# Kernel tuning notes

Hardware: AMD Instinct MI355X
Metric: run time of the kernel (lower is better)

Reference implementation:

```python
import jax, jax.numpy as jnp
import numpy as np
from jax import lax

# Dims from LSTMTagger class constants
B, S, LP = 1024, 128, 14       # sentences, words/sentence, padded chars/word
K, CE, WE, Lf = 3, 6, 10, 4    # char window, char emb, word emb, cnn filters
H, V, A, T = 6, 50000, 100, 135  # lstm hidden, vocab, alphabet, tagset
D = WE + Lf                     # lstm input dim = 14
LW = LP - K + 1                 # conv windows per word = 12


def setup_inputs() -> dict:
    key = jax.random.key(0)
    ks = jax.random.split(key, 14)
    n = lambda k, shp: jax.random.normal(k, shp, dtype=jnp.float32) * 0.1
    inp = {
        "word_idx": jax.random.randint(ks[0], (B, S), 0, V, dtype=jnp.int32),
        "char_idx": jax.random.randint(ks[1], (B, S, LP), 0, A, dtype=jnp.int32),
        "word_emb": n(ks[2], (V, WE)),
        "char_emb": n(ks[3], (A, CE)),
        "Wc": n(ks[4], (Lf, K * CE)),   # Conv1d(1, l, K*CE) weight, squeezed
        "bc": n(ks[5], (Lf,)),
        "Wih_f": n(ks[6], (4 * H, D)),
        "Whh_f": n(ks[7], (4 * H, H)),
        "b_f": n(ks[8], (4 * H,)),      # b_ih + b_hh fused (equivalent)
        "Wih_b": n(ks[9], (4 * H, D)),
        "Whh_b": n(ks[10], (4 * H, H)),
        "b_b": n(ks[11], (4 * H,)),
        "Wt": n(ks[12], (T, 2 * H)),
        "bt": n(ks[13], (T,)),
    }
    return inp


def _lstm_scan(xs, Wih, Whh, b):
    # xs: [S, B, D] -> hs: [S, B, H]; torch gate order i, f, g, o
    h0 = jnp.zeros((xs.shape[1], H), xs.dtype)

    def step(carry, xt):
        h, c = carry
        g = xt @ Wih.T + h @ Whh.T + b
        i, f, gg, o = jnp.split(g, 4, axis=-1)
        c = jax.nn.sigmoid(f) * c + jax.nn.sigmoid(i) * jnp.tanh(gg)
        h = jax.nn.sigmoid(o) * jnp.tanh(c)
        return (h, c), h

    _, hs = lax.scan(step, (h0, h0), xs)
    return hs


def reference(word_emb, char_emb, Wc, bc, Wih_f, Whh_f, b_f,
              Wih_b, Whh_b, b_b, Wt, bt, word_idx, char_idx):
    # per-word char CNN: sliding K-char windows, flatten, linear, max-pool
    ce = char_emb[char_idx]                              # [B,S,LP,CE]
    windows = jnp.concatenate([ce[:, :, i:i + LW] for i in range(K)], axis=-1)  # [B,S,LW,K*CE]
    phi = jnp.einsum('bswk,lk->bswl', windows, Wc) + bc  # [B,S,LW,Lf]
    char_repr = phi.max(axis=2)                          # [B,S,Lf]

    we = word_emb[word_idx]                              # [B,S,WE]
    x = jnp.concatenate([we, char_repr], axis=-1)        # [B,S,D]

    xs = x.transpose(1, 0, 2)                            # [S,B,D]
    hf = _lstm_scan(xs, Wih_f, Whh_f, b_f)               # forward direction
    hb = _lstm_scan(xs[::-1], Wih_b, Whh_b, b_b)[::-1]   # backward direction
    out = jnp.concatenate([hf, hb], axis=-1).transpose(1, 0, 2)  # [B,S,2H]

    tag_space = out @ Wt.T + bt                          # [B,S,T]
    return jax.nn.log_softmax(tag_space, axis=-1)
```

## Files before the change

kernel.cpp:

```cpp
#include <hip/hip_runtime.h>

#define B_   1024
#define S_   128
#define LP_  14
#define K_   3
#define CE_  6
#define WE_  10
#define LF_  4
#define H_   6
#define D_   14
#define T_   135
#define LW_  12
#define V_   50000
#define A_   100
#define SGST 52

static __device__ __forceinline__ float fsigm(float x) {
    return __frcp_rn(1.0f + __expf(-x));
}
static __device__ __forceinline__ float ftanh(float x) {
    return fmaf(2.0f, __frcp_rn(1.0f + __expf(-2.0f * x)), -1.0f);
}

static __device__ __forceinline__ float wave_sum64(float s) {
    int v = __float_as_int(s);
    float f;
    f = __int_as_float(__builtin_amdgcn_update_dpp(0, v, 0xB1, 0xF, 0xF, true));  s += f; v = __float_as_int(s);
    f = __int_as_float(__builtin_amdgcn_update_dpp(0, v, 0x4E, 0xF, 0xF, true));  s += f; v = __float_as_int(s);
    f = __int_as_float(__builtin_amdgcn_update_dpp(0, v, 0x141, 0xF, 0xF, true)); s += f; v = __float_as_int(s);
    f = __int_as_float(__builtin_amdgcn_update_dpp(0, v, 0x140, 0xF, 0xF, true)); s += f; v = __float_as_int(s);
    f = __int_as_float(__builtin_amdgcn_update_dpp(0, v, 0x142, 0xA, 0xF, true)); s += f; v = __float_as_int(s);
    f = __int_as_float(__builtin_amdgcn_update_dpp(0, v, 0x143, 0xC, 0xF, true)); s += f; v = __float_as_int(s);
    return __int_as_float(__builtin_amdgcn_readlane(v, 63));
}

__global__ __launch_bounds__(128, 2) void k_f(
    const int* __restrict__ word_idx, const int* __restrict__ char_idx,
    const float* __restrict__ word_emb, const float* __restrict__ char_emb,
    const float* __restrict__ Wc, const float* __restrict__ bc,
    const float* __restrict__ Wih_f, const float* __restrict__ Whh_f, const float* __restrict__ b_f,
    const float* __restrict__ Wih_b, const float* __restrict__ Whh_b, const float* __restrict__ b_b,
    float* __restrict__ hbuf)
{
    __shared__ __align__(16) float s_g[S_][SGST];
    __shared__ __align__(16) float s_h[S_][12];
    __shared__ float s_ce[A_ * CE_];
    __shared__ float s_wc[LF_ * K_ * CE_];
    __shared__ float s_bc[LF_];

    int t = threadIdx.x;
    int b = blockIdx.x;

    for (int e = t; e < A_ * CE_; e += 128) s_ce[e] = char_emb[e];
    if (t < LF_ * K_ * CE_) s_wc[t] = Wc[t];
    if (t < LF_) s_bc[t] = bc[t];
    __syncthreads();

    {
        int w = b * S_ + t;
        const int2* ci2 = (const int2*)(char_idx + (size_t)w * LP_);
        int idxs[LP_];
        #pragma unroll
        for (int p = 0; p < 7; ++p) {
            int2 v = ci2[p];
            idxs[2 * p] = v.x; idxs[2 * p + 1] = v.y;
        }
        float ce[LP_][CE_];
        #pragma unroll
        for (int p = 0; p < LP_; ++p) {
            int idx = idxs[p];
            idx = idx < 0 ? 0 : (idx >= A_ ? A_ - 1 : idx);
            #pragma unroll
            for (int c = 0; c < CE_; ++c) ce[p][c] = s_ce[idx * CE_ + c];
        }
        float x[D_];
        #pragma unroll
        for (int l = 0; l < LF_; ++l) {
            float acc[LW_];
            float bl = s_bc[l];
            #pragma unroll
            for (int q = 0; q < LW_; ++q) acc[q] = bl;
            #pragma unroll
            for (int kk = 0; kk < K_; ++kk) {
                #pragma unroll
                for (int c = 0; c < CE_; ++c) {
                    float wv_ = s_wc[l * (K_ * CE_) + kk * CE_ + c];
                    #pragma unroll
                    for (int q = 0; q < LW_; ++q) acc[q] = fmaf(ce[q + kk][c], wv_, acc[q]);
                }
            }
            float m = acc[0];
            #pragma unroll
            for (int q = 1; q < LW_; ++q) m = fmaxf(m, acc[q]);
            x[WE_ + l] = m;
        }
        int wi = word_idx[w];
        wi = wi < 0 ? 0 : (wi >= V_ ? V_ - 1 : wi);
        const float2* wep = (const float2*)(word_emb + (size_t)wi * WE_);
        #pragma unroll
        for (int c = 0; c < WE_ / 2; ++c) {
            float2 v = wep[c];
            x[2 * c] = v.x; x[2 * c + 1] = v.y;
        }

        float4* dstf = (float4*)&s_g[t][0];
        {
            float g[24];
            #pragma unroll
            for (int r = 0; r < 24; ++r) {
                float a = b_f[r];
                #pragma unroll
                for (int k = 0; k < D_; ++k) a = fmaf(Wih_f[r * D_ + k], x[k], a);
                g[r] = a;
            }
            #pragma unroll
            for (int u = 0; u < H_; ++u)
                dstf[u] = make_float4(g[u], g[H_ + u], g[2 * H_ + u], g[3 * H_ + u]);
        }
        float4* dstb = (float4*)&s_g[t][24];
        {
            float g[24];
            #pragma unroll
            for (int r = 0; r < 24; ++r) {
                float a = b_b[r];
                #pragma unroll
                for (int k = 0; k < D_; ++k) a = fmaf(Wih_b[r * D_ + k], x[k], a);
                g[r] = a;
            }
            #pragma unroll
            for (int u = 0; u < H_; ++u)
                dstb[u] = make_float4(g[u], g[H_ + u], g[2 * H_ + u], g[3 * H_ + u]);
        }
    }
    __syncthreads();

    {
        int wv   = t >> 6;
        int lane = t & 63;
        bool act = (lane < H_);
        int u    = act ? lane : (H_ - 1);

        const float* Whh = wv ? Whh_b : Whh_f;
        float w0[H_], w1[H_], w2[H_], w3[H_];
        #pragma unroll
        for (int k = 0; k < H_; ++k) {
            w0[k] = Whh[(0 * H_ + u) * H_ + k];
            w1[k] = Whh[(1 * H_ + u) * H_ + k];
            w2[k] = Whh[(2 * H_ + u) * H_ + k];
            w3[k] = Whh[(3 * H_ + u) * H_ + k];
        }

        const float* gp = &s_g[wv ? (S_ - 1) : 0][wv * 24 + u * 4];
        const int gstep = wv ? -SGST : SGST;

        float h[H_];
        #pragma unroll
        for (int k = 0; k < H_; ++k) h[k] = 0.f;
        float c = 0.f;

        float4 g4 = *(const float4*)gp;

#define LSTEP(G4, J)                                                            \
        {                                                                       \
            float ai = (G4).x, af = (G4).y, ag = (G4).z, ao = (G4).w;           \
            _Pragma("unroll")                                                   \
            for (int k = 0; k < H_; ++k) {                                      \
                ai = fmaf(w0[k], h[k], ai);                                     \
                af = fmaf(w1[k], h[k], af);                                     \
                ag = fmaf(w2[k], h[k], ag);                                     \
                ao = fmaf(w3[k], h[k], ao);                                     \
            }                                                                   \
            float si = fsigm(ai), sf = fsigm(af), so = fsigm(ao), tg = ftanh(ag); \
            c = fmaf(sf, c, si * tg);                                           \
            float hu = so * ftanh(c);                                           \
            int se = wv ? (S_ - 1 - (J)) : (J);                                 \
            if (act) s_h[se][wv * H_ + u] = hu;                                 \
            _Pragma("unroll")                                                   \
            for (int k = 0; k < H_; ++k)                                        \
                h[k] = __int_as_float(__builtin_amdgcn_readlane(__float_as_int(hu), k)); \
        }

        #pragma unroll 4
        for (int j = 0; j < S_ - 1; ++j) {
            gp += gstep;
            float4 nx = *(const float4*)gp;
            LSTEP(g4, j);
            g4 = nx;
        }
        LSTEP(g4, S_ - 1);
#undef LSTEP
    }
    __syncthreads();

    {
        float4* dst = (float4*)(hbuf + (size_t)b * S_ * 12);
        const float4* src = (const float4*)&s_h[0][0];
        #pragma unroll
        for (int i = 0; i < 3; ++i) dst[t + 128 * i] = src[t + 128 * i];
    }
}

__global__ __launch_bounds__(256) void k_p(
    const float* __restrict__ hbuf,
    const float* __restrict__ Wt, const float* __restrict__ bt,
    float* __restrict__ out)
{
    __shared__ float s_hb[64 * 12];
    int t = threadIdx.x;
    int ib = blockIdx.x * 64;
    {
        const float4* src = (const float4*)(hbuf + (size_t)ib * 12);
        float4* dst = (float4*)s_hb;
        if (t < 192) dst[t] = src[t];
    }
    __syncthreads();

    int lane = t & 63, wv = t >> 6;
    bool has2 = (lane < T_ - 128);
    int t2c = has2 ? (lane + 128) : (T_ - 1);

    float wA[12], wB[12], wC[12];
    #pragma unroll
    for (int jj = 0; jj < 12; ++jj) {
        wA[jj] = Wt[lane * 12 + jj];
        wB[jj] = Wt[(lane + 64) * 12 + jj];
        wC[jj] = Wt[t2c * 12 + jj];
    }
    float bA = bt[lane], bB = bt[lane + 64], bC = bt[t2c];

    int it0 = wv * 16;
    #pragma unroll 4
    for (int k = 0; k < 16; ++k) {
        int it = it0 + k;
        const float4* h4 = (const float4*)(s_hb + it * 12);
        float4 a0 = h4[0], a1 = h4[1], a2 = h4[2];
        float hv[12] = {a0.x, a0.y, a0.z, a0.w, a1.x, a1.y, a1.z, a1.w, a2.x, a2.y, a2.z, a2.w};
        float y0 = bA, y1 = bB, y2 = bC;
        #pragma unroll
        for (int jj = 0; jj < 12; ++jj) {
            y0 = fmaf(hv[jj], wA[jj], y0);
            y1 = fmaf(hv[jj], wB[jj], y1);
            y2 = fmaf(hv[jj], wC[jj], y2);
        }
        float ss = __expf(y0) + __expf(y1) + (has2 ? __expf(y2) : 0.0f);
        float ls = __logf(wave_sum64(ss));
        float* op = out + (size_t)(ib + it) * T_;
        op[lane]      = y0 - ls;
        op[lane + 64] = y1 - ls;
        if (has2) op[lane + 128] = y2 - ls;
    }
}

extern "C" void kernel_launch(void* const* d_in, const int* in_sizes, int n_in,
                              void* d_out, int out_size, void* d_ws, size_t ws_size,
                              hipStream_t stream)
{
    const int* word_idx = (const int*)d_in[0];
    const int* char_idx = (const int*)d_in[1];
    const float* word_emb = (const float*)d_in[2];
    const float* char_emb = (const float*)d_in[3];
    const float* Wc    = (const float*)d_in[4];
    const float* bc    = (const float*)d_in[5];
    const float* Wih_f = (const float*)d_in[6];
    const float* Whh_f = (const float*)d_in[7];
    const float* b_f   = (const float*)d_in[8];
    const float* Wih_b = (const float*)d_in[9];
    const float* Whh_b = (const float*)d_in[10];
    const float* b_b   = (const float*)d_in[11];
    const float* Wt    = (const float*)d_in[12];
    const float* bt    = (const float*)d_in[13];

    float* hbuf = (float*)d_ws;

    k_f<<<B_, 128, 0, stream>>>(word_idx, char_idx, word_emb, char_emb, Wc, bc,
                                Wih_f, Whh_f, b_f, Wih_b, Whh_b, b_b, hbuf);
    k_p<<<(B_ * S_) / 64, 256, 0, stream>>>(hbuf, Wt, bt, (float*)d_out);
}
```

Baseline: 188.6 us.

## Pack two sentences per LSTM wave using swizzle broadcast within lane groups

Each block now processes two sentences. Each wave runs the recurrence for both at once, with sentence 0 in lanes 0-7 and sentence 1 in lanes 8-15, and the grid is halved. The per-step broadcast of h switches from readlane (a scalar broadcast to the whole wave) to ds_swizzle within 8-lane groups, so each group gets its own sentence's h. The rcp is also swapped for the raw hardware reciprocal. This halves the number of serial recurrence chains per CU, at the cost of doubled shared memory per block, lower occupancy, and possible swizzle latency on the critical path.

```diff
diff --git a/kernel.cpp b/kernel.cpp
--- a/kernel.cpp
+++ b/kernel.cpp
@@ -16,10 +16,10 @@
 #define SGST 52
 
 static __device__ __forceinline__ float fsigm(float x) {
-    return __frcp_rn(1.0f + __expf(-x));
+    return __builtin_amdgcn_rcpf(1.0f + __expf(-x));
 }
 static __device__ __forceinline__ float ftanh(float x) {
-    return fmaf(2.0f, __frcp_rn(1.0f + __expf(-2.0f * x)), -1.0f);
+    return fmaf(2.0f, __builtin_amdgcn_rcpf(1.0f + __expf(-2.0f * x)), -1.0f);
 }
 
 static __device__ __forceinline__ float wave_sum64(float s) {
@@ -34,6 +34,9 @@
     return __int_as_float(__builtin_amdgcn_readlane(v, 63));
 }
 
+#define GBCAST(dst, src, kk) \
+    dst = __int_as_float(__builtin_amdgcn_ds_swizzle(__float_as_int(src), 0x18 | ((kk) << 5)))
+
 __global__ __launch_bounds__(128, 2) void k_f(
     const int* __restrict__ word_idx, const int* __restrict__ char_idx,
     const float* __restrict__ word_emb, const float* __restrict__ char_emb,
@@ -42,22 +45,26 @@
     const float* __restrict__ Wih_b, const float* __restrict__ Whh_b, const float* __restrict__ b_b,
     float* __restrict__ hbuf)
 {
-    __shared__ __align__(16) float s_g[S_][SGST];
-    __shared__ __align__(16) float s_h[S_][12];
+    __shared__ __align__(16) float s_g[2][S_][SGST];
+    __shared__ __align__(16) float s_h[2][S_][12];
     __shared__ float s_ce[A_ * CE_];
     __shared__ float s_wc[LF_ * K_ * CE_];
     __shared__ float s_bc[LF_];
 
     int t = threadIdx.x;
-    int b = blockIdx.x;
+    int blk = blockIdx.x;
 
     for (int e = t; e < A_ * CE_; e += 128) s_ce[e] = char_emb[e];
     if (t < LF_ * K_ * CE_) s_wc[t] = Wc[t];
     if (t < LF_) s_bc[t] = bc[t];
     __syncthreads();
 
-    {
-        int w = b * S_ + t;
+    #pragma unroll
+    for (int rep = 0; rep < 2; ++rep) {
+        int sent = rep;
+        int step = t;
+        int w = (blk * 2 + sent) * S_ + step;
+
         const int2* ci2 = (const int2*)(char_idx + (size_t)w * LP_);
         int idxs[LP_];
         #pragma unroll
@@ -103,7 +110,7 @@
             x[2 * c] = v.x; x[2 * c + 1] = v.y;
         }
 
-        float4* dstf = (float4*)&s_g[t][0];
+        float4* dstf = (float4*)&s_g[sent][step][0];
         {
             float g[24];
             #pragma unroll
@@ -117,7 +124,7 @@
             for (int u = 0; u < H_; ++u)
                 dstf[u] = make_float4(g[u], g[H_ + u], g[2 * H_ + u], g[3 * H_ + u]);
         }
-        float4* dstb = (float4*)&s_g[t][24];
+        float4* dstb = (float4*)&s_g[sent][step][24];
         {
             float g[24];
             #pragma unroll
@@ -135,12 +142,15 @@
     __syncthreads();
 
     {
-        int wv   = t >> 6;
+        int dir  = t >> 6;
         int lane = t & 63;
-        bool act = (lane < H_);
-        int u    = act ? lane : (H_ - 1);
-
-        const float* Whh = wv ? Whh_b : Whh_f;
+        int grp  = lane >> 3;
+        int sent = (grp < 2) ? grp : 1;
+        int u8   = lane & 7;
+        int u    = (u8 < H_) ? u8 : (H_ - 1);
+        bool act = (lane < 16) && (u8 < H_);
+
+        const float* Whh = dir ? Whh_b : Whh_f;
         float w0[H_], w1[H_], w2[H_], w3[H_];
         #pragma unroll
         for (int k = 0; k < H_; ++k) {
@@ -150,8 +160,10 @@
             w3[k] = Whh[(3 * H_ + u) * H_ + k];
         }
 
-        const float* gp = &s_g[wv ? (S_ - 1) : 0][wv * 24 + u * 4];
-        const int gstep = wv ? -SGST : SGST;
+        const float* gp = &s_g[sent][dir ? (S_ - 1) : 0][dir * 24 + u * 4];
+        const int gstep = dir ? -SGST : SGST;
+        float* hp = &s_h[sent][dir ? (S_ - 1) : 0][dir * H_ + u];
+        const int hstep = dir ? -12 : 12;
 
         float h[H_];
         #pragma unroll
@@ -160,7 +172,7 @@
 
         float4 g4 = *(const float4*)gp;
 
-#define LSTEP(G4, J)                                                            \
+#define LSTEP(G4)                                                               \
         {                                                                       \
             float ai = (G4).x, af = (G4).y, ag = (G4).z, ao = (G4).w;           \
             _Pragma("unroll")                                                   \
@@ -173,30 +185,29 @@
             float si = fsigm(ai), sf = fsigm(af), so = fsigm(ao), tg = ftanh(ag); \
             c = fmaf(sf, c, si * tg);                                           \
             float hu = so * ftanh(c);                                           \
-            int se = wv ? (S_ - 1 - (J)) : (J);                                 \
-            if (act) s_h[se][wv * H_ + u] = hu;                                 \
-            _Pragma("unroll")                                                   \
-            for (int k = 0; k < H_; ++k)                                        \
-                h[k] = __int_as_float(__builtin_amdgcn_readlane(__float_as_int(hu), k)); \
+            if (act) *hp = hu;                                                  \
+            hp += hstep;                                                        \
+            GBCAST(h[0], hu, 0); GBCAST(h[1], hu, 1); GBCAST(h[2], hu, 2);      \
+            GBCAST(h[3], hu, 3); GBCAST(h[4], hu, 4); GBCAST(h[5], hu, 5);      \
         }
 
         #pragma unroll 4
         for (int j = 0; j < S_ - 1; ++j) {
             gp += gstep;
             float4 nx = *(const float4*)gp;
-            LSTEP(g4, j);
+            LSTEP(g4);
             g4 = nx;
         }
-        LSTEP(g4, S_ - 1);
+        LSTEP(g4);
 #undef LSTEP
     }
     __syncthreads();
 
     {
-        float4* dst = (float4*)(hbuf + (size_t)b * S_ * 12);
-        const float4* src = (const float4*)&s_h[0][0];
-        #pragma unroll
-        for (int i = 0; i < 3; ++i) dst[t + 128 * i] = src[t + 128 * i];
+        float4* dst = (float4*)(hbuf + (size_t)blk * 2 * S_ * 12);
+        const float4* src = (const float4*)&s_h[0][0][0];
+        #pragma unroll
+        for (int i = 0; i < 6; ++i) dst[t + 128 * i] = src[t + 128 * i];
     }
 }
 
@@ -272,7 +283,7 @@
 
     float* hbuf = (float*)d_ws;
 
-    k_f<<<B_, 128, 0, stream>>>(word_idx, char_idx, word_emb, char_emb, Wc, bc,
-                                Wih_f, Whh_f, b_f, Wih_b, Whh_b, b_b, hbuf);
+    k_f<<<B_ / 2, 128, 0, stream>>>(word_idx, char_idx, word_emb, char_emb, Wc, bc,
+                                    Wih_f, Whh_f, b_f, Wih_b, Whh_b, b_b, hbuf);
     k_p<<<(B_ * S_) / 64, 256, 0, stream>>>(hbuf, Wt, bt, (float*)d_out);
 }
```

Measured after the change: 175.7 us. -6.8%, faster.
